# Kernel optimization log

Measured on AMD Instinct MI355X. Metric: run time of the kernel, lower is better.

Reference implementation:

```python
import jax, jax.numpy as jnp
import numpy as np

N = 100000
E = 1600000
IN_DIM = 128
HID = 128
C = 10
N_INJ = 20000
T_HET = 0.5          # self.hetero_level (set by set_adaptation_from_data)
HP_MAX = 1.0         # highpass_scale_max
INJ_LAM = 0.8        # self.inject_lambda


def setup_inputs() -> dict:
    key = jax.random.key(0)
    ks = jax.random.split(key, 16)
    glorot = lambda k, i, o: jax.random.normal(k, (i, o), jnp.float32) * (2.0 / (i + o)) ** 0.5
    return {
        "x": jax.random.normal(ks[0], (N, IN_DIM), jnp.float32),
        "edge_index": jax.random.randint(ks[1], (2, E), 0, N, jnp.int64),
        "inject_indices": jax.random.randint(ks[2], (N_INJ,), 0, N, jnp.int64),
        "initial_preds": jax.random.uniform(ks[3], (N, C), jnp.float32),
        "W1": glorot(ks[4], IN_DIM, HID), "b1": jnp.zeros((HID,), jnp.float32),
        "W2": glorot(ks[5], HID, HID),   "b2": jnp.zeros((HID,), jnp.float32),
        "Wl1": glorot(ks[6], IN_DIM, HID),
        "Wl2": glorot(ks[7], HID, HID),
        "Wm1": glorot(ks[8], HID, HID), "bm1": jnp.zeros((HID,), jnp.float32),
        "Wm2": glorot(ks[9], HID, C),   "bm2": jnp.zeros((C,), jnp.float32),
    }


def _gcn_norm(edge_index):
    # add self loops, symmetric D^{-1/2} (A+I) D^{-1/2} normalization (PyG GCNConv default)
    loops = jnp.arange(N, dtype=edge_index.dtype)
    src = jnp.concatenate([edge_index[0], loops])
    dst = jnp.concatenate([edge_index[1], loops])
    deg = jax.ops.segment_sum(jnp.ones_like(dst, jnp.float32), dst, num_segments=N)
    dinv = jnp.where(deg > 0, jax.lax.rsqrt(jnp.maximum(deg, 1.0)), 0.0)
    norm = dinv[src] * dinv[dst]  # [E+N]
    return src, dst, norm


def _gcn_conv(x, W, b, src, dst, norm):
    h = x @ W                                   # [N, H]
    msg = h[src] * norm[:, None]                # gather + scale, [E+N, H]
    return jax.ops.segment_sum(msg, dst, num_segments=N) + b


def reference(x, edge_index, inject_indices, initial_preds,
              W1, b1, W2, b2, Wl1, Wl2, Wm1, bm1, Wm2, bm2):
    src, dst, norm = _gcn_norm(edge_index)
    mix = T_HET * HP_MAX

    low1 = _gcn_conv(x, W1, b1, src, dst, norm)
    high1 = x @ Wl1 - low1
    h = jax.nn.relu(low1 + mix * high1)        # dropout: eval mode (identity)

    low2 = _gcn_conv(h, W2, b2, src, dst, norm)
    high2 = h @ Wl2 - low2
    h2 = low2 + mix * high2

    logits = jax.nn.relu(h2 @ Wm1 + bm1) @ Wm2 + bm2   # [N, C]
    # indexed injection: logits[idx] = logits[idx] + lam * preds[idx]
    logits = logits.at[inject_indices].set(
        logits[inject_indices] + INJ_LAM * initial_preds[inject_indices])
    return jax.nn.log_softmax(logits, axis=1)
```

## Files before the change

kernel.cpp:

```cpp
#include <hip/hip_runtime.h>
#include <hip/hip_bf16.h>
#include <math.h>

typedef __attribute__((ext_vector_type(8))) short short8;
typedef __attribute__((ext_vector_type(4))) float f32x4;
typedef __attribute__((ext_vector_type(2))) float f32x2;

#define INJ_LAM 0.8f
#define BSH 9
#define BWD 512

__device__ inline float bf2f(unsigned short s){
  union{unsigned u; float f;} v; v.u=((unsigned)s)<<16; return v.f;
}
__device__ inline unsigned short f2bf(float f){
  __hip_bfloat16 h=__float2bfloat16(f);
  return *reinterpret_cast<unsigned short*>(&h);
}
__device__ inline unsigned pack2(float lo, float hi){
  return ((unsigned)f2bf(hi)<<16)|(unsigned)f2bf(lo);
}

__global__ void k_prep(const float* __restrict__ W1,const float* __restrict__ Wl1,
                       const float* __restrict__ W2,const float* __restrict__ Wl2,
                       const float* __restrict__ Wm1,const float* __restrict__ Wm2,
                       const float* __restrict__ b1,const float* __restrict__ b2,
                       unsigned short* __restrict__ Wt1, unsigned short* __restrict__ Wt2,
                       unsigned short* __restrict__ Wm1t, unsigned short* __restrict__ Wm2tp,
                       float* __restrict__ bh1, float* __restrict__ bh2,
                       unsigned* __restrict__ flags32, int nf4,
                       unsigned* __restrict__ bhist8, unsigned* __restrict__ zcur8){
  int i=blockIdx.x*blockDim.x+threadIdx.x;
  if(i<256*128){
    int c=i>>7, k=i&127;
    float v1=(c<128)?W1[k*128+c]:Wl1[k*128+(c-128)];
    float v2=(c<128)?W2[k*128+c]:Wl2[k*128+(c-128)];
    Wt1[i]=f2bf(v1); Wt2[i]=f2bf(v2);
    if(c<128) Wm1t[i]=f2bf(Wm1[k*128+c]);
    if(c<16)  Wm2tp[i]=f2bf((c<10)?Wm2[k*10+c]:0.f);
    if(i<128){ bh1[i]=0.5f*b1[i]; bh2[i]=0.5f*b2[i]; }
  }
  if(i<nf4) flags32[i]=0u;
  if(i<2048){ bhist8[i]=0u; zcur8[i]=0u; }
}

__global__ void k_bhist(const int* __restrict__ dst, unsigned* __restrict__ bhist8, int E){
  __shared__ unsigned lh[256];
  int t=threadIdx.x;
  lh[t]=0u; __syncthreads();
  int base=blockIdx.x*2048;
  #pragma unroll
  for(int k=0;k<8;k++){
    int e=base+k*256+t;
    if(e<E) atomicAdd(&lh[dst[e]>>BSH],1u);
  }
  __syncthreads();
  if(lh[t]) atomicAdd(&bhist8[t*8],lh[t]);
}

__launch_bounds__(256)
__global__ void k_bscatter(const int* __restrict__ src, const int* __restrict__ dst,
                           const unsigned* __restrict__ bhist8, unsigned* __restrict__ zcur8,
                           int* __restrict__ psrc, int* __restrict__ pdst, int E, int NBK){
  __shared__ unsigned lh[256];
  __shared__ unsigned gb[256];
  __shared__ unsigned ss[256];
  int t=threadIdx.x;
  lh[t]=0u;
  unsigned v=(t<NBK)?bhist8[t*8]:0u;
  ss[t]=v; __syncthreads();
  for(int off=1;off<256;off<<=1){
    unsigned u=(t>=off)?ss[t-off]:0u; __syncthreads();
    ss[t]+=u; __syncthreads();
  }
  unsigned bb=ss[t]-v;
  int base=blockIdx.x*2048;
  unsigned lr[8]; int bk[8], sv[8], dv_[8];
  #pragma unroll
  for(int k=0;k<8;k++){
    int e=base+k*256+t;
    if(e<E){
      int d=dst[e]; int b=d>>BSH;
      bk[k]=b; dv_[k]=d; sv[k]=src[e];
      lr[k]=atomicAdd(&lh[b],1u);
    } else bk[k]=-1;
  }
  __syncthreads();
  if(lh[t]) gb[t]=bb+atomicAdd(&zcur8[t*8],lh[t]);
  __syncthreads();
  #pragma unroll
  for(int k=0;k<8;k++){
    if(bk[k]>=0){
      unsigned p=gb[bk[k]]+lr[k];
      psrc[p]=sv[k]; pdst[p]=dv_[k];
    }
  }
}

__launch_bounds__(256)
__global__ void k_bucket(const int* __restrict__ psrc, const int* __restrict__ pdst,
                         const unsigned* __restrict__ bhist8, unsigned* __restrict__ rank,
                         unsigned* __restrict__ meta, float* __restrict__ dinv,
                         int* __restrict__ csr,
                         const int* __restrict__ inj, unsigned char* __restrict__ flag,
                         int N, int NI, int NBK){
  __shared__ unsigned lc[BWD];
  __shared__ unsigned lo[BWD];
  __shared__ unsigned ss[256];
  int b=blockIdx.x, t=threadIdx.x;
  for(int i=b*256+t;i<NI;i+=gridDim.x*256) flag[inj[i]]=1;
  unsigned v=(t<NBK)?bhist8[t*8]:0u;
  ss[t]=v; lc[t]=0u; lc[t+256]=0u;
  __syncthreads();
  for(int off=1;off<256;off<<=1){
    unsigned u=(t>=off)?ss[t-off]:0u; __syncthreads();
    ss[t]+=u; __syncthreads();
  }
  unsigned e1=ss[b];
  unsigned e0=e1-bhist8[b*8];
  __syncthreads();
  int lo_node=b<<BSH;
  for(unsigned p=e0+t;p<e1;p+=256){
    int dl=pdst[p]-lo_node;
    rank[p]=atomicAdd(&lc[dl],1u);
  }
  __syncthreads();
  unsigned c0=lc[2*t], c1=lc[2*t+1], ps=c0+c1;
  ss[t]=ps; __syncthreads();
  for(int off=1;off<256;off<<=1){
    unsigned u=(t>=off)?ss[t-off]:0u; __syncthreads();
    ss[t]+=u; __syncthreads();
  }
  unsigned excl=ss[t]-ps;
  lo[2*t]=excl; lo[2*t+1]=excl+c0;
  __syncthreads();
  #pragma unroll
  for(int k=0;k<2;k++){
    int nl=t+k*256; int node=lo_node+nl;
    if(node<N){
      unsigned c=lc[nl];
      meta[node]=(e0+lo[nl])|(c<<21);
      dinv[node]=rsqrtf((float)(c+1u));
    }
  }
  for(unsigned p=e0+t;p<e1;p+=256){
    int dl=pdst[p]-lo_node;
    csr[e0+lo[dl]+rank[p]]=psrc[p];
  }
}

template<bool FP32IN>
__device__ inline void load_afrag(const void* __restrict__ Xv, size_t arow, int l4, short8* a){
  if(FP32IN){
    const float* X=(const float*)Xv + arow*128 + l4*8;
    #pragma unroll
    for(int ks=0;ks<4;ks++){
      float4 f0=*reinterpret_cast<const float4*>(X+ks*32);
      float4 f1=*reinterpret_cast<const float4*>(X+ks*32+4);
      short8 t;
      t[0]=(short)f2bf(f0.x); t[1]=(short)f2bf(f0.y); t[2]=(short)f2bf(f0.z); t[3]=(short)f2bf(f0.w);
      t[4]=(short)f2bf(f1.x); t[5]=(short)f2bf(f1.y); t[6]=(short)f2bf(f1.z); t[7]=(short)f2bf(f1.w);
      a[ks]=t;
    }
  }else{
    const unsigned short* X=(const unsigned short*)Xv + arow*128 + l4*8;
    #pragma unroll
    for(int ks=0;ks<4;ks++)
      a[ks]=*reinterpret_cast<const short8*>(X+ks*32);
  }
}

template<bool FP32IN>
__launch_bounds__(256, 4)
__global__ void k_gemm(const void* __restrict__ Xv, const unsigned short* __restrict__ Wt,
                       const float* __restrict__ dinv,
                       unsigned short* __restrict__ G, unsigned short* __restrict__ XL, int N){
  int wave=threadIdx.x>>6, lane=threadIdx.x&63;
  int l15=lane&15, l4=lane>>4;
  int blk0=blockIdx.x*128;
  if(blk0>=N) return;
  short8 wf[4][4];
  #pragma unroll
  for(int i=0;i<4;i++){
    int col=(wave*4+i)*16+l15;
    #pragma unroll
    for(int ks=0;ks<4;ks++)
      wf[i][ks]=*reinterpret_cast<const short8*>(Wt+(size_t)col*128+ks*32+l4*8);
  }
  int r0=blk0+l15; if(r0>N-1) r0=N-1;
  short8 aC[4], aN[4];
  load_afrag<FP32IN>(Xv,(size_t)r0,l4,aC);
  #pragma unroll 1
  for(int nt=0;nt<8;nt++){
    int node0=blk0+nt*16;
    if(node0>=N) break;
    if(nt<7){
      int rn=node0+16+l15; if(rn>N-1) rn=N-1;
      load_afrag<FP32IN>(Xv,(size_t)rn,l4,aN);
    }
    f32x4 acc[4];
    #pragma unroll
    for(int i=0;i<4;i++) acc[i]=(f32x4){0.f,0.f,0.f,0.f};
    #pragma unroll
    for(int i=0;i<4;i++){
      #pragma unroll
      for(int ks=0;ks<4;ks++)
        acc[i]=__builtin_amdgcn_mfma_f32_16x16x32_bf16(wf[i][ks],aC[ks],acc[i],0,0,0);
    }
    int node=node0+l15;
    if(node<N){
      if(wave<2){
        float dv=dinv[node];
        #pragma unroll
        for(int i=0;i<4;i++){
          f32x4 v=acc[i];
          uint2 p; p.x=pack2(v[0]*dv,v[1]*dv); p.y=pack2(v[2]*dv,v[3]*dv);
          *reinterpret_cast<uint2*>(G+(size_t)node*128+(wave*4+i)*16+l4*4)=p;
        }
      }else{
        #pragma unroll
        for(int i=0;i<4;i++){
          f32x4 v=acc[i];
          uint2 p; p.x=pack2(v[0]*0.5f,v[1]*0.5f); p.y=pack2(v[2]*0.5f,v[3]*0.5f);
          *reinterpret_cast<uint2*>(XL+(size_t)node*128+((wave-2)*4+i)*16+l4*4)=p;
        }
      }
    }
    #pragma unroll
    for(int ks=0;ks<4;ks++) aC[ks]=aN[ks];
  }
}

#define ADDQ(v) do{ \
  unsigned ux=(unsigned)(v).x, uy=(unsigned)(v).y, uz=(unsigned)(v).z, uw=(unsigned)(v).w; \
  accv[0]+=(f32x2){__uint_as_float(ux<<16),__uint_as_float(ux&0xffff0000u)}; \
  accv[1]+=(f32x2){__uint_as_float(uy<<16),__uint_as_float(uy&0xffff0000u)}; \
  accv[2]+=(f32x2){__uint_as_float(uz<<16),__uint_as_float(uz&0xffff0000u)}; \
  accv[3]+=(f32x2){__uint_as_float(uw<<16),__uint_as_float(uw&0xffff0000u)}; \
}while(0)

template<bool RELU>
__device__ __forceinline__ void conv_group(int node, int N,
    const unsigned short* __restrict__ G, const unsigned short* __restrict__ XL,
    const float* __restrict__ bh, const float* __restrict__ dinv,
    const int* __restrict__ csr, const unsigned* __restrict__ meta,
    unsigned short* __restrict__ ldsrow, int li){
  if(node>=N) return;
  const int4* Gv=(const int4*)G;
  const int4 Z={0,0,0,0};
  f32x2 accv[4];
  #pragma unroll
  for(int i=0;i<4;i++) accv[i]=(f32x2){0.f,0.f};
  { int4 v=Gv[(size_t)node*16+li]; ADDQ(v); }
  unsigned mt=meta[node];
  unsigned start=mt&0x1FFFFFu, deg=mt>>21;
  int4 v0=Z,v1=Z,v2=Z,v3=Z;
  if(0u<deg) v0=Gv[(size_t)csr[start  ]*16+li];
  if(1u<deg) v1=Gv[(size_t)csr[start+1]*16+li];
  if(2u<deg) v2=Gv[(size_t)csr[start+2]*16+li];
  if(3u<deg) v3=Gv[(size_t)csr[start+3]*16+li];
  unsigned j=4;
  while(j<deg){
    int4 n0=Gv[(size_t)csr[start+j]*16+li];
    int4 n1=(j+1<deg)?Gv[(size_t)csr[start+j+1]*16+li]:Z;
    int4 n2=(j+2<deg)?Gv[(size_t)csr[start+j+2]*16+li]:Z;
    int4 n3=(j+3<deg)?Gv[(size_t)csr[start+j+3]*16+li]:Z;
    ADDQ(v0); ADDQ(v1); ADDQ(v2); ADDQ(v3);
    v0=n0; v1=n1; v2=n2; v3=n3; j+=4;
  }
  ADDQ(v0); ADDQ(v1); ADDQ(v2); ADDQ(v3);
  float acc[8];
  #pragma unroll
  for(int i=0;i<4;i++){ acc[2*i]=accv[i][0]; acc[2*i+1]=accv[i][1]; }
  float dv2=0.5f*dinv[node];
  float4 b0=*reinterpret_cast<const float4*>(bh+li*8);
  float4 b1=*reinterpret_cast<const float4*>(bh+li*8+4);
  int4 xv=((const int4*)XL)[(size_t)node*16+li];
  float xl[8];
  { unsigned _x=(unsigned)xv.x,_y=(unsigned)xv.y,_z=(unsigned)xv.z,_w=(unsigned)xv.w;
    xl[0]=bf2f((unsigned short)(_x&0xffffu)); xl[1]=bf2f((unsigned short)(_x>>16));
    xl[2]=bf2f((unsigned short)(_y&0xffffu)); xl[3]=bf2f((unsigned short)(_y>>16));
    xl[4]=bf2f((unsigned short)(_z&0xffffu)); xl[5]=bf2f((unsigned short)(_z>>16));
    xl[6]=bf2f((unsigned short)(_w&0xffffu)); xl[7]=bf2f((unsigned short)(_w>>16)); }
  float bb[8]={b0.x,b0.y,b0.z,b0.w,b1.x,b1.y,b1.z,b1.w};
  float r[8];
  #pragma unroll
  for(int i=0;i<8;i++){
    r[i]=dv2*acc[i]+bb[i]+xl[i];
    if(RELU) r[i]=fmaxf(r[i],0.f);
  }
  int4 o;
  o.x=(int)pack2(r[0],r[1]); o.y=(int)pack2(r[2],r[3]);
  o.z=(int)pack2(r[4],r[5]); o.w=(int)pack2(r[6],r[7]);
  *reinterpret_cast<int4*>(ldsrow+li*8)=o;
}

__launch_bounds__(256, 6)
__global__ void k_convg(const unsigned short* __restrict__ G1, const unsigned short* __restrict__ XL1,
                        const float* __restrict__ bh1, const float* __restrict__ dinv,
                        const int* __restrict__ csr, const unsigned* __restrict__ meta,
                        const unsigned short* __restrict__ Wt2,
                        unsigned short* __restrict__ G2, unsigned short* __restrict__ XL2, int N){
  __shared__ __align__(16) unsigned short ht[16][136];
  int wave=threadIdx.x>>6, lane=threadIdx.x&63;
  int l15=lane&15, l4=lane>>4;
  int blk0=blockIdx.x*16;
  int nl=wave*4+l4;
  conv_group<true>(blk0+nl, N, G1, XL1, bh1, dinv, csr, meta, &ht[nl][0], l15);
  __syncthreads();
  short8 a[4];
  #pragma unroll
  for(int ks=0;ks<4;ks++)
    a[ks]=*reinterpret_cast<const short8*>(&ht[l15][ks*32+l4*8]);
  int node=blk0+l15;
  float dv=(node<N)?dinv[node]:0.f;
  #pragma unroll
  for(int i=0;i<4;i++){
    int ct=wave*4+i;
    short8 wfr[4];
    #pragma unroll
    for(int ks=0;ks<4;ks++)
      wfr[ks]=*reinterpret_cast<const short8*>(Wt2+(size_t)(ct*16+l15)*128+ks*32+l4*8);
    f32x4 acc=(f32x4){0.f,0.f,0.f,0.f};
    #pragma unroll
    for(int ks=0;ks<4;ks++)
      acc=__builtin_amdgcn_mfma_f32_16x16x32_bf16(wfr[ks],a[ks],acc,0,0,0);
    if(node<N){
      if(ct<8){
        uint2 p; p.x=pack2(acc[0]*dv,acc[1]*dv); p.y=pack2(acc[2]*dv,acc[3]*dv);
        *reinterpret_cast<uint2*>(G2+(size_t)node*128+ct*16+l4*4)=p;
      }else{
        uint2 p; p.x=pack2(acc[0]*0.5f,acc[1]*0.5f); p.y=pack2(acc[2]*0.5f,acc[3]*0.5f);
        *reinterpret_cast<uint2*>(XL2+(size_t)node*128+(ct-8)*16+l4*4)=p;
      }
    }
  }
}

__launch_bounds__(256, 6)
__global__ void k_convm(const unsigned short* __restrict__ G2, const unsigned short* __restrict__ XL2,
                        const float* __restrict__ bh2, const float* __restrict__ dinv,
                        const int* __restrict__ csr, const unsigned* __restrict__ meta,
                        const unsigned short* __restrict__ Wm1t, const unsigned short* __restrict__ Wm2tp,
                        const float* __restrict__ bm1, const float* __restrict__ bm2,
                        const unsigned char* __restrict__ flag, const float* __restrict__ preds,
                        float* __restrict__ out, int N){
  __shared__ __align__(16) unsigned short ht[16][136];
  __shared__ __align__(16) unsigned short zt[16][136];
  int wave=threadIdx.x>>6, lane=threadIdx.x&63;
  int l15=lane&15, l4=lane>>4;
  int blk0=blockIdx.x*16;
  int nl=wave*4+l4;
  conv_group<false>(blk0+nl, N, G2, XL2, bh2, dinv, csr, meta, &ht[nl][0], l15);
  __syncthreads();
  short8 a[4];
  #pragma unroll
  for(int ks=0;ks<4;ks++)
    a[ks]=*reinterpret_cast<const short8*>(&ht[l15][ks*32+l4*8]);
  #pragma unroll
  for(int i=0;i<2;i++){
    int ct=wave*2+i;
    short8 wfr[4];
    #pragma unroll
    for(int ks=0;ks<4;ks++)
      wfr[ks]=*reinterpret_cast<const short8*>(Wm1t+(size_t)(ct*16+l15)*128+ks*32+l4*8);
    f32x4 acc=(f32x4){0.f,0.f,0.f,0.f};
    #pragma unroll
    for(int ks=0;ks<4;ks++)
      acc=__builtin_amdgcn_mfma_f32_16x16x32_bf16(wfr[ks],a[ks],acc,0,0,0);
    float4 bm=*reinterpret_cast<const float4*>(bm1+ct*16+l4*4);
    uint2 p;
    p.x=pack2(fmaxf(acc[0]+bm.x,0.f),fmaxf(acc[1]+bm.y,0.f));
    p.y=pack2(fmaxf(acc[2]+bm.z,0.f),fmaxf(acc[3]+bm.w,0.f));
    *reinterpret_cast<uint2*>(&zt[l15][ct*16+l4*4])=p;
  }
  __syncthreads();
  if(wave==0){
    short8 a2[4], w2[4];
    #pragma unroll
    for(int ks=0;ks<4;ks++){
      a2[ks]=*reinterpret_cast<const short8*>(&zt[l15][ks*32+l4*8]);
      w2[ks]=*reinterpret_cast<const short8*>(Wm2tp+(size_t)l15*128+ks*32+l4*8);
    }
    f32x4 acc2=(f32x4){0.f,0.f,0.f,0.f};
    #pragma unroll
    for(int ks=0;ks<4;ks++)
      acc2=__builtin_amdgcn_mfma_f32_16x16x32_bf16(w2[ks],a2[ks],acc2,0,0,0);
    int node=blk0+l15;
    bool have=node<N;
    int c0=l4*4;
    float v[4];
    #pragma unroll
    for(int k=0;k<4;k++){
      int c=c0+k;
      v[k]=(c<10)?(acc2[k]+bm2[c]):-3.0e38f;
    }
    if(have && c0<10 && flag[node]){
      #pragma unroll
      for(int k=0;k<4;k++){
        int c=c0+k;
        if(c<10) v[k]+=INJ_LAM*preds[(size_t)node*10+c];
      }
    }
    float m=fmaxf(fmaxf(v[0],v[1]),fmaxf(v[2],v[3]));
    m=fmaxf(m,__shfl_xor(m,16,64));
    m=fmaxf(m,__shfl_xor(m,32,64));
    float s=0.f;
    #pragma unroll
    for(int k=0;k<4;k++){ int c=c0+k; if(c<10) s+=expf(v[k]-m); }
    s+=__shfl_xor(s,16,64);
    s+=__shfl_xor(s,32,64);
    float lse=m+logf(s);
    if(have && c0<10){
      float2 o01; o01.x=v[0]-lse; o01.y=v[1]-lse;
      *reinterpret_cast<float2*>(out+(size_t)node*10+c0)=o01;
      if(c0+2<10){
        float2 o23; o23.x=v[2]-lse; o23.y=v[3]-lse;
        *reinterpret_cast<float2*>(out+(size_t)node*10+c0+2)=o23;
      }
    }
  }
}

extern "C" void kernel_launch(void* const* d_in, const int* in_sizes, int n_in,
                              void* d_out, int out_size, void* d_ws, size_t ws_size,
                              hipStream_t stream){
  const float* x    =(const float*)d_in[0];
  const int*   ei   =(const int*)  d_in[1];
  const int*   inj  =(const int*)  d_in[2];
  const float* preds=(const float*)d_in[3];
  const float* W1 =(const float*)d_in[4];  const float* b1 =(const float*)d_in[5];
  const float* W2 =(const float*)d_in[6];  const float* b2 =(const float*)d_in[7];
  const float* Wl1=(const float*)d_in[8];  const float* Wl2=(const float*)d_in[9];
  const float* Wm1=(const float*)d_in[10]; const float* bm1=(const float*)d_in[11];
  const float* Wm2=(const float*)d_in[12]; const float* bm2=(const float*)d_in[13];
  float* out=(float*)d_out;

  const int N  = in_sizes[0]/128;
  const int E  = in_sizes[1]/2;
  const int NI = in_sizes[2];
  const int* srcp = ei;
  const int* dstp = ei+E;
  const int NBK = (N+BWD-1)>>BSH;

  char* w=(char*)d_ws;
  auto carve=[&](size_t sz)->char*{ char* p=w; w+=(sz+255)&~(size_t)255; return p; };
  unsigned short* S1 =(unsigned short*)carve((size_t)N*128*2);
  unsigned short* S2 =(unsigned short*)carve((size_t)N*128*2);
  unsigned short* S3 =(unsigned short*)carve((size_t)N*128*2);
  unsigned short* Wt1=(unsigned short*)carve(256*128*2);
  unsigned short* Wt2=(unsigned short*)carve(256*128*2);
  unsigned short* Wm1t=(unsigned short*)carve(128*128*2);
  unsigned short* Wm2tp=(unsigned short*)carve(16*128*2);
  float*    dinv  =(float*)   carve((size_t)N*4);
  unsigned* meta  =(unsigned*)carve((size_t)N*4);
  int*      csr   =(int*)     carve((size_t)E*4);
  unsigned char* flags=(unsigned char*)carve(((size_t)N+3)&~(size_t)3);
  unsigned* bhist8=(unsigned*)carve(256*8*4);
  unsigned* zcur8 =(unsigned*)carve(256*8*4);
  float* bh1=(float*)carve(128*4);
  float* bh2=(float*)carve(128*4);
  (void)ws_size; (void)n_in; (void)out_size;

  int* psrc=(int*)S3;
  int* pdst=psrc+E;
  unsigned* rank=(unsigned*)S1;

  const int T=256;
  const int EB=(E+2047)/2048;
  const int nf4=(N+3)/4;
  int gp=(32768>nf4?32768:nf4); gp=(gp+T-1)/T;
  hipLaunchKernelGGL(k_prep, dim3(gp), dim3(T), 0, stream,
                     W1,Wl1,W2,Wl2,Wm1,Wm2,b1,b2,
                     Wt1,Wt2,Wm1t,Wm2tp,bh1,bh2,
                     (unsigned*)flags, nf4, bhist8, zcur8);
  hipLaunchKernelGGL(k_bhist, dim3(EB), dim3(T), 0, stream, dstp, bhist8, E);
  hipLaunchKernelGGL(k_bscatter, dim3(EB), dim3(T), 0, stream, srcp, dstp, bhist8, zcur8,
                     psrc, pdst, E, NBK);
  hipLaunchKernelGGL(k_bucket, dim3(NBK), dim3(T), 0, stream, psrc, pdst, bhist8, rank,
                     meta, dinv, csr, inj, flags, N, NI, NBK);
  hipLaunchKernelGGL(k_gemm<true>, dim3((N+127)/128), dim3(T), 0, stream,
                     (const void*)x, Wt1, dinv, S1, S2, N);
  hipLaunchKernelGGL(k_convg, dim3((N+15)/16), dim3(T), 0, stream,
                     S1, S2, bh1, dinv, csr, meta, Wt2, S2, S3, N);
  hipLaunchKernelGGL(k_convm, dim3((N+15)/16), dim3(T), 0, stream,
                     S2, S3, bh2, dinv, csr, meta, Wm1t, Wm2tp, bm1, bm2,
                     flags, preds, out, N);
}
```

Measured before the change: 327.4 us.

## Assign one wave per node in conv kernels with 4-way neighbor split

Each conv kernel now uses 1024-thread blocks in which every wave aggregates one node. The four 16-lane groups of a wave take interleaved neighbors and combine their partial sums with cross-lane shuffles. Previously each 16-lane group handled a whole node. The follow-on MFMA work is redistributed so each wave computes a single 16-column tile. The aim is more memory-level parallelism per node on the irregular gathers and a shorter per-node dependency chain. In exchange it adds shuffle overhead, larger blocks and barriers over 16 waves, and may lower occupancy.

After: 373.6 us. +14.1%, slower.

```diff
diff --git a/kernel.cpp b/kernel.cpp
--- a/kernel.cpp
+++ b/kernel.cpp
@@ -240,62 +240,74 @@
 }while(0)
 
 template<bool RELU>
-__device__ __forceinline__ void conv_group(int node, int N,
+__device__ __forceinline__ void conv_node(int node, int N,
     const unsigned short* __restrict__ G, const unsigned short* __restrict__ XL,
     const float* __restrict__ bh, const float* __restrict__ dinv,
     const int* __restrict__ csr, const unsigned* __restrict__ meta,
-    unsigned short* __restrict__ ldsrow, int li){
+    unsigned short* __restrict__ ldsrow, int lane){
   if(node>=N) return;
+  int g=lane>>4, li=lane&15;
   const int4* Gv=(const int4*)G;
   const int4 Z={0,0,0,0};
   f32x2 accv[4];
   #pragma unroll
   for(int i=0;i<4;i++) accv[i]=(f32x2){0.f,0.f};
-  { int4 v=Gv[(size_t)node*16+li]; ADDQ(v); }
+  if(g==0){
+    int4 v=Gv[(size_t)node*16+li];
+    ADDQ(v);
+  }
   unsigned mt=meta[node];
   unsigned start=mt&0x1FFFFFu, deg=mt>>21;
+  unsigned j=(unsigned)g;
   int4 v0=Z,v1=Z,v2=Z,v3=Z;
-  if(0u<deg) v0=Gv[(size_t)csr[start  ]*16+li];
-  if(1u<deg) v1=Gv[(size_t)csr[start+1]*16+li];
-  if(2u<deg) v2=Gv[(size_t)csr[start+2]*16+li];
-  if(3u<deg) v3=Gv[(size_t)csr[start+3]*16+li];
-  unsigned j=4;
+  if(j<deg)    v0=Gv[(size_t)csr[start+j]*16+li];
+  if(j+4<deg)  v1=Gv[(size_t)csr[start+j+4]*16+li];
+  if(j+8<deg)  v2=Gv[(size_t)csr[start+j+8]*16+li];
+  if(j+12<deg) v3=Gv[(size_t)csr[start+j+12]*16+li];
+  j+=16;
   while(j<deg){
     int4 n0=Gv[(size_t)csr[start+j]*16+li];
-    int4 n1=(j+1<deg)?Gv[(size_t)csr[start+j+1]*16+li]:Z;
-    int4 n2=(j+2<deg)?Gv[(size_t)csr[start+j+2]*16+li]:Z;
-    int4 n3=(j+3<deg)?Gv[(size_t)csr[start+j+3]*16+li]:Z;
+    int4 n1=(j+4<deg)?Gv[(size_t)csr[start+j+4]*16+li]:Z;
+    int4 n2=(j+8<deg)?Gv[(size_t)csr[start+j+8]*16+li]:Z;
+    int4 n3=(j+12<deg)?Gv[(size_t)csr[start+j+12]*16+li]:Z;
     ADDQ(v0); ADDQ(v1); ADDQ(v2); ADDQ(v3);
-    v0=n0; v1=n1; v2=n2; v3=n3; j+=4;
+    v0=n0; v1=n1; v2=n2; v3=n3; j+=16;
   }
   ADDQ(v0); ADDQ(v1); ADDQ(v2); ADDQ(v3);
   float acc[8];
   #pragma unroll
   for(int i=0;i<4;i++){ acc[2*i]=accv[i][0]; acc[2*i+1]=accv[i][1]; }
-  float dv2=0.5f*dinv[node];
-  float4 b0=*reinterpret_cast<const float4*>(bh+li*8);
-  float4 b1=*reinterpret_cast<const float4*>(bh+li*8+4);
-  int4 xv=((const int4*)XL)[(size_t)node*16+li];
-  float xl[8];
-  { unsigned _x=(unsigned)xv.x,_y=(unsigned)xv.y,_z=(unsigned)xv.z,_w=(unsigned)xv.w;
-    xl[0]=bf2f((unsigned short)(_x&0xffffu)); xl[1]=bf2f((unsigned short)(_x>>16));
-    xl[2]=bf2f((unsigned short)(_y&0xffffu)); xl[3]=bf2f((unsigned short)(_y>>16));
-    xl[4]=bf2f((unsigned short)(_z&0xffffu)); xl[5]=bf2f((unsigned short)(_z>>16));
-    xl[6]=bf2f((unsigned short)(_w&0xffffu)); xl[7]=bf2f((unsigned short)(_w>>16)); }
-  float bb[8]={b0.x,b0.y,b0.z,b0.w,b1.x,b1.y,b1.z,b1.w};
-  float r[8];
   #pragma unroll
   for(int i=0;i<8;i++){
-    r[i]=dv2*acc[i]+bb[i]+xl[i];
-    if(RELU) r[i]=fmaxf(r[i],0.f);
-  }
-  int4 o;
-  o.x=(int)pack2(r[0],r[1]); o.y=(int)pack2(r[2],r[3]);
-  o.z=(int)pack2(r[4],r[5]); o.w=(int)pack2(r[6],r[7]);
-  *reinterpret_cast<int4*>(ldsrow+li*8)=o;
-}
-
-__launch_bounds__(256, 6)
+    acc[i]+=__shfl_xor(acc[i],16,64);
+    acc[i]+=__shfl_xor(acc[i],32,64);
+  }
+  if(g==0){
+    float dv2=0.5f*dinv[node];
+    float4 b0=*reinterpret_cast<const float4*>(bh+li*8);
+    float4 b1=*reinterpret_cast<const float4*>(bh+li*8+4);
+    int4 xv=((const int4*)XL)[(size_t)node*16+li];
+    float xl[8];
+    { unsigned _x=(unsigned)xv.x,_y=(unsigned)xv.y,_z=(unsigned)xv.z,_w=(unsigned)xv.w;
+      xl[0]=bf2f((unsigned short)(_x&0xffffu)); xl[1]=bf2f((unsigned short)(_x>>16));
+      xl[2]=bf2f((unsigned short)(_y&0xffffu)); xl[3]=bf2f((unsigned short)(_y>>16));
+      xl[4]=bf2f((unsigned short)(_z&0xffffu)); xl[5]=bf2f((unsigned short)(_z>>16));
+      xl[6]=bf2f((unsigned short)(_w&0xffffu)); xl[7]=bf2f((unsigned short)(_w>>16)); }
+    float bb[8]={b0.x,b0.y,b0.z,b0.w,b1.x,b1.y,b1.z,b1.w};
+    float r[8];
+    #pragma unroll
+    for(int i=0;i<8;i++){
+      r[i]=dv2*acc[i]+bb[i]+xl[i];
+      if(RELU) r[i]=fmaxf(r[i],0.f);
+    }
+    int4 o;
+    o.x=(int)pack2(r[0],r[1]); o.y=(int)pack2(r[2],r[3]);
+    o.z=(int)pack2(r[4],r[5]); o.w=(int)pack2(r[6],r[7]);
+    *reinterpret_cast<int4*>(ldsrow+li*8)=o;
+  }
+}
+
+__launch_bounds__(1024)
 __global__ void k_convg(const unsigned short* __restrict__ G1, const unsigned short* __restrict__ XL1,
                         const float* __restrict__ bh1, const float* __restrict__ dinv,
                         const int* __restrict__ csr, const unsigned* __restrict__ meta,
@@ -305,39 +317,32 @@
   int wave=threadIdx.x>>6, lane=threadIdx.x&63;
   int l15=lane&15, l4=lane>>4;
   int blk0=blockIdx.x*16;
-  int nl=wave*4+l4;
-  conv_group<true>(blk0+nl, N, G1, XL1, bh1, dinv, csr, meta, &ht[nl][0], l15);
-  __syncthreads();
-  short8 a[4];
+  conv_node<true>(blk0+wave, N, G1, XL1, bh1, dinv, csr, meta, &ht[wave][0], lane);
+  __syncthreads();
+  short8 wfr[4], a[4];
+  #pragma unroll
+  for(int ks=0;ks<4;ks++){
+    wfr[ks]=*reinterpret_cast<const short8*>(Wt2+(size_t)(wave*16+l15)*128+ks*32+l4*8);
+    a[ks]=*reinterpret_cast<const short8*>(&ht[l15][ks*32+l4*8]);
+  }
+  f32x4 acc=(f32x4){0.f,0.f,0.f,0.f};
   #pragma unroll
   for(int ks=0;ks<4;ks++)
-    a[ks]=*reinterpret_cast<const short8*>(&ht[l15][ks*32+l4*8]);
+    acc=__builtin_amdgcn_mfma_f32_16x16x32_bf16(wfr[ks],a[ks],acc,0,0,0);
   int node=blk0+l15;
-  float dv=(node<N)?dinv[node]:0.f;
-  #pragma unroll
-  for(int i=0;i<4;i++){
-    int ct=wave*4+i;
-    short8 wfr[4];
-    #pragma unroll
-    for(int ks=0;ks<4;ks++)
-      wfr[ks]=*reinterpret_cast<const short8*>(Wt2+(size_t)(ct*16+l15)*128+ks*32+l4*8);
-    f32x4 acc=(f32x4){0.f,0.f,0.f,0.f};
-    #pragma unroll
-    for(int ks=0;ks<4;ks++)
-      acc=__builtin_amdgcn_mfma_f32_16x16x32_bf16(wfr[ks],a[ks],acc,0,0,0);
-    if(node<N){
-      if(ct<8){
-        uint2 p; p.x=pack2(acc[0]*dv,acc[1]*dv); p.y=pack2(acc[2]*dv,acc[3]*dv);
-        *reinterpret_cast<uint2*>(G2+(size_t)node*128+ct*16+l4*4)=p;
-      }else{
-        uint2 p; p.x=pack2(acc[0]*0.5f,acc[1]*0.5f); p.y=pack2(acc[2]*0.5f,acc[3]*0.5f);
-        *reinterpret_cast<uint2*>(XL2+(size_t)node*128+(ct-8)*16+l4*4)=p;
-      }
-    }
-  }
-}
-
-__launch_bounds__(256, 6)
+  if(node<N){
+    if(wave<8){
+      float dv=dinv[node];
+      uint2 p; p.x=pack2(acc[0]*dv,acc[1]*dv); p.y=pack2(acc[2]*dv,acc[3]*dv);
+      *reinterpret_cast<uint2*>(G2+(size_t)node*128+wave*16+l4*4)=p;
+    }else{
+      uint2 p; p.x=pack2(acc[0]*0.5f,acc[1]*0.5f); p.y=pack2(acc[2]*0.5f,acc[3]*0.5f);
+      *reinterpret_cast<uint2*>(XL2+(size_t)node*128+(wave-8)*16+l4*4)=p;
+    }
+  }
+}
+
+__launch_bounds__(1024)
 __global__ void k_convm(const unsigned short* __restrict__ G2, const unsigned short* __restrict__ XL2,
                         const float* __restrict__ bh2, const float* __restrict__ dinv,
                         const int* __restrict__ csr, const unsigned* __restrict__ meta,
@@ -350,20 +355,16 @@
   int wave=threadIdx.x>>6, lane=threadIdx.x&63;
   int l15=lane&15, l4=lane>>4;
   int blk0=blockIdx.x*16;
-  int nl=wave*4+l4;
-  conv_group<false>(blk0+nl, N, G2, XL2, bh2, dinv, csr, meta, &ht[nl][0], l15);
-  __syncthreads();
-  short8 a[4];
-  #pragma unroll
-  for(int ks=0;ks<4;ks++)
-    a[ks]=*reinterpret_cast<const short8*>(&ht[l15][ks*32+l4*8]);
-  #pragma unroll
-  for(int i=0;i<2;i++){
-    int ct=wave*2+i;
-    short8 wfr[4];
-    #pragma unroll
-    for(int ks=0;ks<4;ks++)
+  conv_node<false>(blk0+wave, N, G2, XL2, bh2, dinv, csr, meta, &ht[wave][0], lane);
+  __syncthreads();
+  if(wave<8){
+    int ct=wave;
+    short8 wfr[4], a[4];
+    #pragma unroll
+    for(int ks=0;ks<4;ks++){
       wfr[ks]=*reinterpret_cast<const short8*>(Wm1t+(size_t)(ct*16+l15)*128+ks*32+l4*8);
+      a[ks]=*reinterpret_cast<const short8*>(&ht[l15][ks*32+l4*8]);
+    }
     f32x4 acc=(f32x4){0.f,0.f,0.f,0.f};
     #pragma unroll
     for(int ks=0;ks<4;ks++)
@@ -481,9 +482,9 @@
                      meta, dinv, csr, inj, flags, N, NI, NBK);
   hipLaunchKernelGGL(k_gemm<true>, dim3((N+127)/128), dim3(T), 0, stream,
                      (const void*)x, Wt1, dinv, S1, S2, N);
-  hipLaunchKernelGGL(k_convg, dim3((N+15)/16), dim3(T), 0, stream,
+  hipLaunchKernelGGL(k_convg, dim3((N+15)/16), dim3(1024), 0, stream,
                      S1, S2, bh1, dinv, csr, meta, Wt2, S2, S3, N);
-  hipLaunchKernelGGL(k_convm, dim3((N+15)/16), dim3(T), 0, stream,
+  hipLaunchKernelGGL(k_convm, dim3((N+15)/16), dim3(1024), 0, stream,
                      S2, S3, bh2, dinv, csr, meta, Wm1t, Wm2tp, bm1, bm2,
                      flags, preds, out, N);
 }
```

## Sort nodes by in-degree to balance per-wave aggregation work in conv kernels

Applied to the files above, without the earlier changes.

Builds a degree histogram in the bucket kernel and adds a counting-sort kernel that produces a node permutation grouped by in-degree. Both conv kernels then process nodes in permuted order, so nodes sharing a wave have similar neighbour counts and lanes idle less during the gather loop. The cost is an extra kernel launch, an indirection load per node, and scattered rather than contiguous output row writes.

New measurement: 337.0 us. +2.9%, slower.

```diff
diff --git a/kernel.cpp b/kernel.cpp
--- a/kernel.cpp
+++ b/kernel.cpp
@@ -29,7 +29,8 @@
                        unsigned short* __restrict__ Wm1t, unsigned short* __restrict__ Wm2tp,
                        float* __restrict__ bh1, float* __restrict__ bh2,
                        unsigned* __restrict__ flags32, int nf4,
-                       unsigned* __restrict__ bhist8, unsigned* __restrict__ zcur8){
+                       unsigned* __restrict__ bhist8, unsigned* __restrict__ zcur8,
+                       unsigned* __restrict__ dhist8, unsigned* __restrict__ dcur8){
   int i=blockIdx.x*blockDim.x+threadIdx.x;
   if(i<256*128){
     int c=i>>7, k=i&127;
@@ -42,6 +43,7 @@
   }
   if(i<nf4) flags32[i]=0u;
   if(i<2048){ bhist8[i]=0u; zcur8[i]=0u; }
+  if(i<512){ dhist8[i]=0u; dcur8[i]=0u; }
 }
 
 __global__ void k_bhist(const int* __restrict__ dst, unsigned* __restrict__ bhist8, int E){
@@ -103,14 +105,17 @@
                          unsigned* __restrict__ meta, float* __restrict__ dinv,
                          int* __restrict__ csr,
                          const int* __restrict__ inj, unsigned char* __restrict__ flag,
+                         unsigned* __restrict__ dhist8,
                          int N, int NI, int NBK){
   __shared__ unsigned lc[BWD];
   __shared__ unsigned lo[BWD];
   __shared__ unsigned ss[256];
+  __shared__ unsigned dh[64];
   int b=blockIdx.x, t=threadIdx.x;
   for(int i=b*256+t;i<NI;i+=gridDim.x*256) flag[inj[i]]=1;
   unsigned v=(t<NBK)?bhist8[t*8]:0u;
   ss[t]=v; lc[t]=0u; lc[t+256]=0u;
+  if(t<64) dh[t]=0u;
   __syncthreads();
   for(int off=1;off<256;off<<=1){
     unsigned u=(t>=off)?ss[t-off]:0u; __syncthreads();
@@ -141,12 +146,42 @@
       unsigned c=lc[nl];
       meta[node]=(e0+lo[nl])|(c<<21);
       dinv[node]=rsqrtf((float)(c+1u));
+      unsigned bin=c; if(bin>63u) bin=63u;
+      atomicAdd(&dh[bin],1u);
     }
   }
   for(unsigned p=e0+t;p<e1;p+=256){
     int dl=pdst[p]-lo_node;
     csr[e0+lo[dl]+rank[p]]=psrc[p];
   }
+  __syncthreads();
+  if(t<64 && dh[t]) atomicAdd(&dhist8[t*8],dh[t]);
+}
+
+__launch_bounds__(256)
+__global__ void k_perm(const unsigned* __restrict__ meta,
+                       const unsigned* __restrict__ dhist8, unsigned* __restrict__ dcur8,
+                       int* __restrict__ perm, int N){
+  __shared__ unsigned base[64];
+  __shared__ unsigned lh[64];
+  __shared__ unsigned gb[64];
+  int t=threadIdx.x;
+  if(t<64){
+    unsigned s=0;
+    for(int j=0;j<t;j++) s+=dhist8[j*8];
+    base[t]=s; lh[t]=0u;
+  }
+  __syncthreads();
+  int i=blockIdx.x*256+t;
+  unsigned d=0, lr=0;
+  if(i<N){
+    d=meta[i]>>21; if(d>63u) d=63u;
+    lr=atomicAdd(&lh[d],1u);
+  }
+  __syncthreads();
+  if(t<64 && lh[t]) gb[t]=atomicAdd(&dcur8[t*8],lh[t]);
+  __syncthreads();
+  if(i<N) perm[base[d]+gb[d]+lr]=i;
 }
 
 template<bool FP32IN>
@@ -299,6 +334,7 @@
 __global__ void k_convg(const unsigned short* __restrict__ G1, const unsigned short* __restrict__ XL1,
                         const float* __restrict__ bh1, const float* __restrict__ dinv,
                         const int* __restrict__ csr, const unsigned* __restrict__ meta,
+                        const int* __restrict__ perm,
                         const unsigned short* __restrict__ Wt2,
                         unsigned short* __restrict__ G2, unsigned short* __restrict__ XL2, int N){
   __shared__ __align__(16) unsigned short ht[16][136];
@@ -306,14 +342,17 @@
   int l15=lane&15, l4=lane>>4;
   int blk0=blockIdx.x*16;
   int nl=wave*4+l4;
-  conv_group<true>(blk0+nl, N, G1, XL1, bh1, dinv, csr, meta, &ht[nl][0], l15);
+  int idx=blk0+nl;
+  int node=(idx<N)?perm[idx]:N;
+  conv_group<true>(node, N, G1, XL1, bh1, dinv, csr, meta, &ht[nl][0], l15);
   __syncthreads();
   short8 a[4];
   #pragma unroll
   for(int ks=0;ks<4;ks++)
     a[ks]=*reinterpret_cast<const short8*>(&ht[l15][ks*32+l4*8]);
-  int node=blk0+l15;
-  float dv=(node<N)?dinv[node]:0.f;
+  int idx2=blk0+l15;
+  int onode=(idx2<N)?perm[idx2]:-1;
+  float dv=(onode>=0)?dinv[onode]:0.f;
   #pragma unroll
   for(int i=0;i<4;i++){
     int ct=wave*4+i;
@@ -325,13 +364,13 @@
     #pragma unroll
     for(int ks=0;ks<4;ks++)
       acc=__builtin_amdgcn_mfma_f32_16x16x32_bf16(wfr[ks],a[ks],acc,0,0,0);
-    if(node<N){
+    if(onode>=0){
       if(ct<8){
         uint2 p; p.x=pack2(acc[0]*dv,acc[1]*dv); p.y=pack2(acc[2]*dv,acc[3]*dv);
-        *reinterpret_cast<uint2*>(G2+(size_t)node*128+ct*16+l4*4)=p;
+        *reinterpret_cast<uint2*>(G2+(size_t)onode*128+ct*16+l4*4)=p;
       }else{
         uint2 p; p.x=pack2(acc[0]*0.5f,acc[1]*0.5f); p.y=pack2(acc[2]*0.5f,acc[3]*0.5f);
-        *reinterpret_cast<uint2*>(XL2+(size_t)node*128+(ct-8)*16+l4*4)=p;
+        *reinterpret_cast<uint2*>(XL2+(size_t)onode*128+(ct-8)*16+l4*4)=p;
       }
     }
   }
@@ -341,6 +380,7 @@
 __global__ void k_convm(const unsigned short* __restrict__ G2, const unsigned short* __restrict__ XL2,
                         const float* __restrict__ bh2, const float* __restrict__ dinv,
                         const int* __restrict__ csr, const unsigned* __restrict__ meta,
+                        const int* __restrict__ perm,
                         const unsigned short* __restrict__ Wm1t, const unsigned short* __restrict__ Wm2tp,
                         const float* __restrict__ bm1, const float* __restrict__ bm2,
                         const unsigned char* __restrict__ flag, const float* __restrict__ preds,
@@ -351,7 +391,9 @@
   int l15=lane&15, l4=lane>>4;
   int blk0=blockIdx.x*16;
   int nl=wave*4+l4;
-  conv_group<false>(blk0+nl, N, G2, XL2, bh2, dinv, csr, meta, &ht[nl][0], l15);
+  int idx=blk0+nl;
+  int node=(idx<N)?perm[idx]:N;
+  conv_group<false>(node, N, G2, XL2, bh2, dinv, csr, meta, &ht[nl][0], l15);
   __syncthreads();
   short8 a[4];
   #pragma unroll
@@ -386,8 +428,9 @@
     #pragma unroll
     for(int ks=0;ks<4;ks++)
       acc2=__builtin_amdgcn_mfma_f32_16x16x32_bf16(w2[ks],a2[ks],acc2,0,0,0);
-    int node=blk0+l15;
-    bool have=node<N;
+    int idx2=blk0+l15;
+    int onode=(idx2<N)?perm[idx2]:-1;
+    bool have=onode>=0;
     int c0=l4*4;
     float v[4];
     #pragma unroll
@@ -395,11 +438,11 @@
       int c=c0+k;
       v[k]=(c<10)?(acc2[k]+bm2[c]):-3.0e38f;
     }
-    if(have && c0<10 && flag[node]){
+    if(have && c0<10 && flag[onode]){
       #pragma unroll
       for(int k=0;k<4;k++){
         int c=c0+k;
-        if(c<10) v[k]+=INJ_LAM*preds[(size_t)node*10+c];
+        if(c<10) v[k]+=INJ_LAM*preds[(size_t)onode*10+c];
       }
     }
     float m=fmaxf(fmaxf(v[0],v[1]),fmaxf(v[2],v[3]));
@@ -413,10 +456,10 @@
     float lse=m+logf(s);
     if(have && c0<10){
       float2 o01; o01.x=v[0]-lse; o01.y=v[1]-lse;
-      *reinterpret_cast<float2*>(out+(size_t)node*10+c0)=o01;
+      *reinterpret_cast<float2*>(out+(size_t)onode*10+c0)=o01;
       if(c0+2<10){
         float2 o23; o23.x=v[2]-lse; o23.y=v[3]-lse;
-        *reinterpret_cast<float2*>(out+(size_t)node*10+c0+2)=o23;
+        *reinterpret_cast<float2*>(out+(size_t)onode*10+c0+2)=o23;
       }
     }
   }
@@ -458,6 +501,9 @@
   unsigned char* flags=(unsigned char*)carve(((size_t)N+3)&~(size_t)3);
   unsigned* bhist8=(unsigned*)carve(256*8*4);
   unsigned* zcur8 =(unsigned*)carve(256*8*4);
+  unsigned* dhist8=(unsigned*)carve(64*8*4);
+  unsigned* dcur8 =(unsigned*)carve(64*8*4);
+  int*      perm  =(int*)carve((size_t)N*4);
   float* bh1=(float*)carve(128*4);
   float* bh2=(float*)carve(128*4);
   (void)ws_size; (void)n_in; (void)out_size;
@@ -473,17 +519,18 @@
   hipLaunchKernelGGL(k_prep, dim3(gp), dim3(T), 0, stream,
                      W1,Wl1,W2,Wl2,Wm1,Wm2,b1,b2,
                      Wt1,Wt2,Wm1t,Wm2tp,bh1,bh2,
-                     (unsigned*)flags, nf4, bhist8, zcur8);
+                     (unsigned*)flags, nf4, bhist8, zcur8, dhist8, dcur8);
   hipLaunchKernelGGL(k_bhist, dim3(EB), dim3(T), 0, stream, dstp, bhist8, E);
   hipLaunchKernelGGL(k_bscatter, dim3(EB), dim3(T), 0, stream, srcp, dstp, bhist8, zcur8,
                      psrc, pdst, E, NBK);
   hipLaunchKernelGGL(k_bucket, dim3(NBK), dim3(T), 0, stream, psrc, pdst, bhist8, rank,
-                     meta, dinv, csr, inj, flags, N, NI, NBK);
+                     meta, dinv, csr, inj, flags, dhist8, N, NI, NBK);
+  hipLaunchKernelGGL(k_perm, dim3((N+T-1)/T), dim3(T), 0, stream, meta, dhist8, dcur8, perm, N);
   hipLaunchKernelGGL(k_gemm<true>, dim3((N+127)/128), dim3(T), 0, stream,
                      (const void*)x, Wt1, dinv, S1, S2, N);
   hipLaunchKernelGGL(k_convg, dim3((N+15)/16), dim3(T), 0, stream,
-                     S1, S2, bh1, dinv, csr, meta, Wt2, S2, S3, N);
+                     S1, S2, bh1, dinv, csr, meta, perm, Wt2, S2, S3, N);
   hipLaunchKernelGGL(k_convm, dim3((N+15)/16), dim3(T), 0, stream,
-                     S2, S3, bh2, dinv, csr, meta, Wm1t, Wm2tp, bm1, bm2,
+                     S2, S3, bh2, dinv, csr, meta, perm, Wm1t, Wm2tp, bm1, bm2,
                      flags, preds, out, N);
 }
```

## Drop histogram pass with fixed-capacity buckets, deepen gather unroll, raise occupancy

Applied to the files above, without the earlier changes.

Removes the separate destination-bucket histogram kernel by scattering edges into fixed-capacity bucket slots (BCAP per bucket), with the running atomic counter doubling as the bucket count for the later prefix sum. The neighbor gather in the GCN conv loop now keeps eight loads in flight instead of four, and the conv kernels request higher occupancy through launch bounds. The fixed capacity assumes no bucket of 512 destination nodes receives more than 12288 edges, which holds for uniformly random graphs but would overflow silently on skewed degree distributions. The added registers from the deeper unroll may also conflict with the higher occupancy target.

Result: slower. 659.8 us (+101.5%).

```diff
diff --git a/kernel.cpp b/kernel.cpp
--- a/kernel.cpp
+++ b/kernel.cpp
@@ -9,6 +9,7 @@
 #define INJ_LAM 0.8f
 #define BSH 9
 #define BWD 512
+#define BCAP 12288
 
 __device__ inline float bf2f(unsigned short s){
   union{unsigned u; float f;} v; v.u=((unsigned)s)<<16; return v.f;
@@ -29,7 +30,7 @@
                        unsigned short* __restrict__ Wm1t, unsigned short* __restrict__ Wm2tp,
                        float* __restrict__ bh1, float* __restrict__ bh2,
                        unsigned* __restrict__ flags32, int nf4,
-                       unsigned* __restrict__ bhist8, unsigned* __restrict__ zcur8){
+                       unsigned* __restrict__ zcur8){
   int i=blockIdx.x*blockDim.x+threadIdx.x;
   if(i<256*128){
     int c=i>>7, k=i&127;
@@ -41,39 +42,17 @@
     if(i<128){ bh1[i]=0.5f*b1[i]; bh2[i]=0.5f*b2[i]; }
   }
   if(i<nf4) flags32[i]=0u;
-  if(i<2048){ bhist8[i]=0u; zcur8[i]=0u; }
-}
-
-__global__ void k_bhist(const int* __restrict__ dst, unsigned* __restrict__ bhist8, int E){
+  if(i<2048) zcur8[i]=0u;
+}
+
+__launch_bounds__(256)
+__global__ void k_bscatter(const int* __restrict__ src, const int* __restrict__ dst,
+                           unsigned* __restrict__ zcur8,
+                           int* __restrict__ psrc, int* __restrict__ pdst, int E){
   __shared__ unsigned lh[256];
+  __shared__ unsigned gb[256];
   int t=threadIdx.x;
   lh[t]=0u; __syncthreads();
-  int base=blockIdx.x*2048;
-  #pragma unroll
-  for(int k=0;k<8;k++){
-    int e=base+k*256+t;
-    if(e<E) atomicAdd(&lh[dst[e]>>BSH],1u);
-  }
-  __syncthreads();
-  if(lh[t]) atomicAdd(&bhist8[t*8],lh[t]);
-}
-
-__launch_bounds__(256)
-__global__ void k_bscatter(const int* __restrict__ src, const int* __restrict__ dst,
-                           const unsigned* __restrict__ bhist8, unsigned* __restrict__ zcur8,
-                           int* __restrict__ psrc, int* __restrict__ pdst, int E, int NBK){
-  __shared__ unsigned lh[256];
-  __shared__ unsigned gb[256];
-  __shared__ unsigned ss[256];
-  int t=threadIdx.x;
-  lh[t]=0u;
-  unsigned v=(t<NBK)?bhist8[t*8]:0u;
-  ss[t]=v; __syncthreads();
-  for(int off=1;off<256;off<<=1){
-    unsigned u=(t>=off)?ss[t-off]:0u; __syncthreads();
-    ss[t]+=u; __syncthreads();
-  }
-  unsigned bb=ss[t]-v;
   int base=blockIdx.x*2048;
   unsigned lr[8]; int bk[8], sv[8], dv_[8];
   #pragma unroll
@@ -86,12 +65,12 @@
     } else bk[k]=-1;
   }
   __syncthreads();
-  if(lh[t]) gb[t]=bb+atomicAdd(&zcur8[t*8],lh[t]);
+  if(lh[t]) gb[t]=atomicAdd(&zcur8[t*8],lh[t]);
   __syncthreads();
   #pragma unroll
   for(int k=0;k<8;k++){
     if(bk[k]>=0){
-      unsigned p=gb[bk[k]]+lr[k];
+      unsigned p=(unsigned)bk[k]*BCAP+gb[bk[k]]+lr[k];
       psrc[p]=sv[k]; pdst[p]=dv_[k];
     }
   }
@@ -99,7 +78,7 @@
 
 __launch_bounds__(256)
 __global__ void k_bucket(const int* __restrict__ psrc, const int* __restrict__ pdst,
-                         const unsigned* __restrict__ bhist8, unsigned* __restrict__ rank,
+                         const unsigned* __restrict__ zcur8, unsigned* __restrict__ rank,
                          unsigned* __restrict__ meta, float* __restrict__ dinv,
                          int* __restrict__ csr,
                          const int* __restrict__ inj, unsigned char* __restrict__ flag,
@@ -109,20 +88,22 @@
   __shared__ unsigned ss[256];
   int b=blockIdx.x, t=threadIdx.x;
   for(int i=b*256+t;i<NI;i+=gridDim.x*256) flag[inj[i]]=1;
-  unsigned v=(t<NBK)?bhist8[t*8]:0u;
+  unsigned v=(t<NBK)?zcur8[t*8]:0u;
   ss[t]=v; lc[t]=0u; lc[t+256]=0u;
   __syncthreads();
   for(int off=1;off<256;off<<=1){
     unsigned u=(t>=off)?ss[t-off]:0u; __syncthreads();
     ss[t]+=u; __syncthreads();
   }
+  unsigned cnt_b=zcur8[b*8];
   unsigned e1=ss[b];
-  unsigned e0=e1-bhist8[b*8];
+  unsigned e0=e1-cnt_b;
   __syncthreads();
   int lo_node=b<<BSH;
-  for(unsigned p=e0+t;p<e1;p+=256){
-    int dl=pdst[p]-lo_node;
-    rank[p]=atomicAdd(&lc[dl],1u);
+  unsigned pbase=(unsigned)b*BCAP;
+  for(unsigned i=t;i<cnt_b;i+=256){
+    int dl=pdst[pbase+i]-lo_node;
+    rank[pbase+i]=atomicAdd(&lc[dl],1u);
   }
   __syncthreads();
   unsigned c0=lc[2*t], c1=lc[2*t+1], ps=c0+c1;
@@ -143,9 +124,9 @@
       dinv[node]=rsqrtf((float)(c+1u));
     }
   }
-  for(unsigned p=e0+t;p<e1;p+=256){
-    int dl=pdst[p]-lo_node;
-    csr[e0+lo[dl]+rank[p]]=psrc[p];
+  for(unsigned i=t;i<cnt_b;i+=256){
+    int dl=pdst[pbase+i]-lo_node;
+    csr[e0+lo[dl]+rank[pbase+i]]=psrc[pbase+i];
   }
 }
 
@@ -254,21 +235,32 @@
   { int4 v=Gv[(size_t)node*16+li]; ADDQ(v); }
   unsigned mt=meta[node];
   unsigned start=mt&0x1FFFFFu, deg=mt>>21;
-  int4 v0=Z,v1=Z,v2=Z,v3=Z;
+  int4 v0=Z,v1=Z,v2=Z,v3=Z,v4=Z,v5=Z,v6=Z,v7=Z;
   if(0u<deg) v0=Gv[(size_t)csr[start  ]*16+li];
   if(1u<deg) v1=Gv[(size_t)csr[start+1]*16+li];
   if(2u<deg) v2=Gv[(size_t)csr[start+2]*16+li];
   if(3u<deg) v3=Gv[(size_t)csr[start+3]*16+li];
-  unsigned j=4;
+  if(4u<deg) v4=Gv[(size_t)csr[start+4]*16+li];
+  if(5u<deg) v5=Gv[(size_t)csr[start+5]*16+li];
+  if(6u<deg) v6=Gv[(size_t)csr[start+6]*16+li];
+  if(7u<deg) v7=Gv[(size_t)csr[start+7]*16+li];
+  unsigned j=8;
   while(j<deg){
     int4 n0=Gv[(size_t)csr[start+j]*16+li];
     int4 n1=(j+1<deg)?Gv[(size_t)csr[start+j+1]*16+li]:Z;
     int4 n2=(j+2<deg)?Gv[(size_t)csr[start+j+2]*16+li]:Z;
     int4 n3=(j+3<deg)?Gv[(size_t)csr[start+j+3]*16+li]:Z;
+    int4 n4=(j+4<deg)?Gv[(size_t)csr[start+j+4]*16+li]:Z;
+    int4 n5=(j+5<deg)?Gv[(size_t)csr[start+j+5]*16+li]:Z;
+    int4 n6=(j+6<deg)?Gv[(size_t)csr[start+j+6]*16+li]:Z;
+    int4 n7=(j+7<deg)?Gv[(size_t)csr[start+j+7]*16+li]:Z;
     ADDQ(v0); ADDQ(v1); ADDQ(v2); ADDQ(v3);
-    v0=n0; v1=n1; v2=n2; v3=n3; j+=4;
+    ADDQ(v4); ADDQ(v5); ADDQ(v6); ADDQ(v7);
+    v0=n0; v1=n1; v2=n2; v3=n3; v4=n4; v5=n5; v6=n6; v7=n7;
+    j+=8;
   }
   ADDQ(v0); ADDQ(v1); ADDQ(v2); ADDQ(v3);
+  ADDQ(v4); ADDQ(v5); ADDQ(v6); ADDQ(v7);
   float acc[8];
   #pragma unroll
   for(int i=0;i<4;i++){ acc[2*i]=accv[i][0]; acc[2*i+1]=accv[i][1]; }
@@ -295,7 +287,7 @@
   *reinterpret_cast<int4*>(ldsrow+li*8)=o;
 }
 
-__launch_bounds__(256, 6)
+__launch_bounds__(256, 8)
 __global__ void k_convg(const unsigned short* __restrict__ G1, const unsigned short* __restrict__ XL1,
                         const float* __restrict__ bh1, const float* __restrict__ dinv,
                         const int* __restrict__ csr, const unsigned* __restrict__ meta,
@@ -337,7 +329,7 @@
   }
 }
 
-__launch_bounds__(256, 6)
+__launch_bounds__(256, 8)
 __global__ void k_convm(const unsigned short* __restrict__ G2, const unsigned short* __restrict__ XL2,
                         const float* __restrict__ bh2, const float* __restrict__ dinv,
                         const int* __restrict__ csr, const unsigned* __restrict__ meta,
@@ -456,14 +448,13 @@
   unsigned* meta  =(unsigned*)carve((size_t)N*4);
   int*      csr   =(int*)     carve((size_t)E*4);
   unsigned char* flags=(unsigned char*)carve(((size_t)N+3)&~(size_t)3);
-  unsigned* bhist8=(unsigned*)carve(256*8*4);
   unsigned* zcur8 =(unsigned*)carve(256*8*4);
   float* bh1=(float*)carve(128*4);
   float* bh2=(float*)carve(128*4);
   (void)ws_size; (void)n_in; (void)out_size;
 
   int* psrc=(int*)S3;
-  int* pdst=psrc+E;
+  int* pdst=psrc+(size_t)NBK*BCAP;
   unsigned* rank=(unsigned*)S1;
 
   const int T=256;
@@ -473,11 +464,10 @@
   hipLaunchKernelGGL(k_prep, dim3(gp), dim3(T), 0, stream,
                      W1,Wl1,W2,Wl2,Wm1,Wm2,b1,b2,
                      Wt1,Wt2,Wm1t,Wm2tp,bh1,bh2,
-                     (unsigned*)flags, nf4, bhist8, zcur8);
-  hipLaunchKernelGGL(k_bhist, dim3(EB), dim3(T), 0, stream, dstp, bhist8, E);
-  hipLaunchKernelGGL(k_bscatter, dim3(EB), dim3(T), 0, stream, srcp, dstp, bhist8, zcur8,
-                     psrc, pdst, E, NBK);
-  hipLaunchKernelGGL(k_bucket, dim3(NBK), dim3(T), 0, stream, psrc, pdst, bhist8, rank,
+                     (unsigned*)flags, nf4, zcur8);
+  hipLaunchKernelGGL(k_bscatter, dim3(EB), dim3(T), 0, stream, srcp, dstp, zcur8,
+                     psrc, pdst, E);
+  hipLaunchKernelGGL(k_bucket, dim3(NBK), dim3(T), 0, stream, psrc, pdst, zcur8, rank,
                      meta, dinv, csr, inj, flags, N, NI, NBK);
   hipLaunchKernelGGL(k_gemm<true>, dim3((N+127)/128), dim3(T), 0, stream,
                      (const void*)x, Wt1, dinv, S1, S2, N);
```
